# Optimization experiments

Measured on AMD Instinct MI355X. Metric: run time of the kernel, lower is better.

The kernel has to match this reference:

```python
import jax, jax.numpy as jnp
import numpy as np

N_EMBD = 1024
N_HEAD = 16
HEAD_DIM = N_EMBD // N_HEAD


def setup_inputs() -> dict:
    key = jax.random.key(0)
    k1, k2, k3 = jax.random.split(key, 3)
    x = jax.random.normal(k1, (2, 2048, N_EMBD), dtype=jnp.float32)
    # torch nn.Linear(in, out) weight has shape (out, in); y = x @ W.T
    w_qkv = jax.random.normal(k2, (3 * N_EMBD, N_EMBD), dtype=jnp.float32) * (1.0 / np.sqrt(N_EMBD))
    w_proj = jax.random.normal(k3, (N_EMBD, N_EMBD), dtype=jnp.float32) * (1.0 / np.sqrt(N_EMBD))
    return {"x": x, "w_qkv": w_qkv, "w_proj": w_proj}


def reference(x, w_qkv, w_proj):
    B, T, C = x.shape
    qkv = jnp.einsum('btc,dc->btd', x, w_qkv)  # [B,T,3C]
    q, k, v = jnp.split(qkv, 3, axis=2)
    # [B,H,T,hd]
    q = q.reshape(B, T, N_HEAD, HEAD_DIM).transpose(0, 2, 1, 3)
    k = k.reshape(B, T, N_HEAD, HEAD_DIM).transpose(0, 2, 1, 3)
    v = v.reshape(B, T, N_HEAD, HEAD_DIM).transpose(0, 2, 1, 3)
    att = jnp.einsum('bhqd,bhkd->bhqk', q, k) / jnp.sqrt(jnp.float32(HEAD_DIM))
    causal = jnp.tril(jnp.ones((T, T), dtype=bool))  # [T,T]
    att = jnp.where(causal[None, None], att, -jnp.inf)
    att = jax.nn.softmax(att, axis=-1)
    y = jnp.einsum('bhqk,bhkd->bhqd', att, v)
    y = y.transpose(0, 2, 1, 3).reshape(B, T, C)
    return jnp.einsum('btc,dc->btd', y, w_proj)
```

## Files before the change

kernel.cpp:

```cpp
#include <hip/hip_runtime.h>
#include <stdint.h>


typedef unsigned short u16;
typedef __bf16 bf16_t;
typedef bf16_t bf16x8 __attribute__((ext_vector_type(8)));
typedef float f32x4 __attribute__((ext_vector_type(4)));
typedef float f32x16 __attribute__((ext_vector_type(16)));

__device__ __forceinline__ u16 f2bf(float f) {
  return __builtin_bit_cast(u16, (bf16_t)f);
}

__device__ __forceinline__ float hexp2(float x) {
  float r;
  asm("v_exp_f32 %0, %1" : "=v"(r) : "v"(x));
  return r;
}
__device__ __forceinline__ uint32_t cvtpk(float lo, float hi) {
  uint32_t d;
  asm("v_cvt_pk_bf16_f32 %0, %1, %2" : "=v"(d) : "v"(lo), "v"(hi));
  return d;
}
__device__ __forceinline__ void plswap(uint32_t& a, uint32_t& b) {
  asm("v_permlane32_swap_b32 %0, %1" : "+v"(a), "+v"(b));
}

template<int CC>
__device__ __forceinline__ bf16x8 mkPfrag(const float* p) {
  uint32_t A1 = cvtpk(p[8 * CC + 0], p[8 * CC + 1]);
  uint32_t A2 = cvtpk(p[8 * CC + 2], p[8 * CC + 3]);
  uint32_t B1 = cvtpk(p[8 * CC + 4], p[8 * CC + 5]);
  uint32_t B2 = cvtpk(p[8 * CC + 6], p[8 * CC + 7]);
  plswap(A1, B1);
  plswap(A2, B2);
  union { uint32_t u[4]; bf16x8 v; } r;
  r.u[0] = A1; r.u[1] = A2; r.u[2] = B1; r.u[3] = B2;
  return r.v;
}

__device__ __forceinline__ void gload_lds16(const void* g, void* l) {
  __builtin_amdgcn_global_load_lds(
      (const __attribute__((address_space(1))) uint32_t*)(uint64_t)g,
      (__attribute__((address_space(3))) uint32_t*)(uint32_t)(uint64_t)l,
      16, 0, 0);
}

__global__ void cast_all(const float* __restrict__ x, const float* __restrict__ wq,
                         const float* __restrict__ wp, u16* __restrict__ xb,
                         u16* __restrict__ wqb, u16* __restrict__ wpb) {
  int i = blockIdx.x * blockDim.x + threadIdx.x;
  const float* s; u16* d; int off;
  if (i < 1048576)            { s = x;  d = xb;  off = i; }
  else if (i < 1048576 + 786432) { s = wq; d = wqb; off = i - 1048576; }
  else                        { s = wp; d = wpb; off = i - (1048576 + 786432); }
  float4 f = reinterpret_cast<const float4*>(s)[off];
  ushort4 o;
  o.x = f2bf(f.x); o.y = f2bf(f.y); o.z = f2bf(f.z); o.w = f2bf(f.w);
  reinterpret_cast<ushort4*>(d)[off] = o;
}

template<int MODE>
__global__ void gemm_bt(const u16* __restrict__ A, const u16* __restrict__ Bm,
                        u16* __restrict__ qb, u16* __restrict__ kb, u16* __restrict__ vb,
                        float* __restrict__ outf) {
  __shared__ __attribute__((aligned(16))) u16 SMEM[2 * 128 * 64];
  const int tid = threadIdx.x;
  const int lane = tid & 63;
  const int w = tid >> 6;
  const int wr = w >> 1, wc = w & 1;
  const int g = lane >> 4, r = lane & 15;
  const int tn = blockIdx.x, tm = blockIdx.y;

  f32x4 acc[4][4] = {};

  const char* Ab = (const char*)(A + (size_t)tm * 128 * 1024);
  const char* Bb = (const char*)(Bm + (size_t)tn * 128 * 1024);
  char* AsB = (char*)SMEM;
  char* BsB = AsB + 16384;

  for (int k0 = 0; k0 < 1024; k0 += 64) {
#pragma unroll
    for (int i = 0; i < 4; ++i) {
      const int L = (i * 256 + tid) * 16;
      const int row = L >> 7;
      const int colb = (L & 127) ^ ((row & 7) << 4);
      gload_lds16(Ab + (size_t)row * 2048 + k0 * 2 + colb, AsB + L);
      gload_lds16(Bb + (size_t)row * 2048 + k0 * 2 + colb, BsB + L);
    }
    __syncthreads();
#pragma unroll
    for (int kk = 0; kk < 2; ++kk) {
      bf16x8 a[4], b[4];
#pragma unroll
      for (int m = 0; m < 4; ++m) {
        const int rowA = wr * 64 + m * 16 + r;
        const int kbyt = (kk * 64 + g * 16) ^ ((rowA & 7) << 4);
        a[m] = *(const bf16x8*)(AsB + rowA * 128 + kbyt);
      }
#pragma unroll
      for (int n = 0; n < 4; ++n) {
        const int rowB = wc * 64 + n * 16 + r;
        const int kbyt = (kk * 64 + g * 16) ^ ((rowB & 7) << 4);
        b[n] = *(const bf16x8*)(BsB + rowB * 128 + kbyt);
      }
      __builtin_amdgcn_s_setprio(1);
#pragma unroll
      for (int m = 0; m < 4; ++m)
#pragma unroll
        for (int n = 0; n < 4; ++n)
          acc[m][n] = __builtin_amdgcn_mfma_f32_16x16x32_bf16(a[m], b[n], acc[m][n], 0, 0, 0);
      __builtin_amdgcn_s_setprio(0);
    }
    __syncthreads();
  }

  const int mrow0 = tm * 128 + wr * 64;
  const int ncol0 = tn * 128 + wc * 64;

  if (MODE == 1) {
#pragma unroll
    for (int m = 0; m < 4; ++m)
#pragma unroll
      for (int n = 0; n < 4; ++n) {
        const int nc = ncol0 + n * 16 + r;
#pragma unroll
        for (int j = 0; j < 4; ++j) {
          const int mr = mrow0 + m * 16 + g * 4 + j;
          outf[(size_t)mr * 1024 + nc] = acc[m][n][j];
        }
      }
  } else {
    const int sel = (blockIdx.x * 128) >> 10;
    const float qscl = (sel == 0) ? 0.18033688f : 1.0f;
    if (sel < 2) {
      u16* dst = (sel == 0) ? qb : kb;
#pragma unroll
      for (int m = 0; m < 4; ++m)
#pragma unroll
        for (int n = 0; n < 4; ++n) {
          const int nc = (ncol0 + n * 16 + r) & 1023;
          const int h = nc >> 6, d = nc & 63;
#pragma unroll
          for (int j = 0; j < 4; ++j) {
            const int mr = mrow0 + m * 16 + g * 4 + j;
            const int bb = mr >> 11, t = mr & 2047;
            dst[((size_t)(bb * 16 + h) * 2048 + t) * 64 + d] = f2bf(acc[m][n][j] * qscl);
          }
        }
    } else {
      u16* Wv = SMEM + w * 4096;
#pragma unroll
      for (int m = 0; m < 4; ++m)
#pragma unroll
        for (int n = 0; n < 4; ++n) {
          const int dl = n * 16 + r;
          uint32_t lo = cvtpk(acc[m][n][0], acc[m][n][1]);
          uint32_t hi2 = cvtpk(acc[m][n][2], acc[m][n][3]);
          char* p = (char*)Wv + dl * 128 + ((m * 32 + g * 8) ^ ((dl & 7) << 4));
          *(uint32_t*)p = lo;
          *(uint32_t*)(p + 4) = hi2;
        }
      asm volatile("s_waitcnt lgkmcnt(0)" ::: "memory");
      __builtin_amdgcn_sched_barrier(0);
      const int hh = (ncol0 - 2048) >> 6;
      const int t0 = mrow0 & 2047;
      const int bb2 = mrow0 >> 11;
      u16* vdst = vb + ((size_t)(bb2 * 16 + hh) * 64) * 2048 + t0;
#pragma unroll
      for (int rd = 0; rd < 8; ++rd) {
        const int dl = rd * 8 + (lane >> 3);
        const int tb = lane & 7;
        const char* src = (char*)Wv + dl * 128 + ((tb ^ (dl & 7)) << 4);
        *(uint4*)(vdst + (size_t)dl * 2048 + tb * 8) = *(const uint4*)src;
      }
    }
  }
}

__global__ __launch_bounds__(256, 2)
void attn_fwd(const u16* __restrict__ qb, const u16* __restrict__ kb,
              const u16* __restrict__ vb, u16* __restrict__ yb) {
  __shared__ __attribute__((aligned(16))) u16 KV[2][2][64 * 64];
  __shared__ __attribute__((aligned(16))) float Linv[4][32];
  const int tid = threadIdx.x;
  const int lane = tid & 63;
  const int w = tid >> 6;
  const int hi = lane >> 5;
  const int q5 = lane & 31;
  const int hi4 = hi * 4;
  const int bh = blockIdx.x;
  const int bb = bh >> 4, h = bh & 15;
  const int base = (blockIdx.y + bh) & 15;
  const int a = (base < 8) ? 2 * base : 31 - 2 * base;
  const int qb0 = a * 128;
  const int qw = qb0 + w * 32;
  const int qg = qw + q5;

  const char* Kb = (const char*)(kb + (size_t)bh * (2048 * 64));
  const char* Vb = (const char*)(vb + (size_t)bh * (64 * 2048));
  const u16* Q = qb + (size_t)bh * (2048 * 64);

  bf16x8 qf[4];
#pragma unroll
  for (int f = 0; f < 4; ++f)
    qf[f] = *(const bf16x8*)(&Q[(size_t)qg * 64 + f * 16 + hi * 8]);

  f32x16 o0 = {}, o1 = {};
  float psum = 0.0f;

  const int nt = (qw >> 6) + 1;
  const int ntmax = (qb0 >> 6) + 2;
  const int swz = (q5 & 7) << 4;

  auto stage = [&](int k0, int buf) {
#pragma unroll
    for (int i = 0; i < 2; ++i) {
      const int L = (i * 256 + tid) * 16;
      const int row = L >> 7;
      const int colb = (L & 127) ^ ((row & 7) << 4);
      gload_lds16(Kb + (size_t)(k0 + row) * 128 + colb, (char*)KV[buf][0] + L);
      gload_lds16(Vb + (size_t)row * 4096 + (size_t)k0 * 2 + colb,
                  (char*)KV[buf][1] + L);
    }
  };

  auto compute = [&](int t, int k0, const char* KsB, const char* VsB) {
    f32x16 s0 = {}, s1 = {};
    __builtin_amdgcn_s_setprio(1);
#pragma unroll
    for (int f = 0; f < 4; ++f) {
      const int cb = f * 32 + hi * 16;
      bf16x8 ka0 = *(const bf16x8*)(KsB + q5 * 128 + (cb ^ swz));
      bf16x8 ka1 = *(const bf16x8*)(KsB + (32 + q5) * 128 + (cb ^ swz));
      s0 = __builtin_amdgcn_mfma_f32_32x32x16_bf16(ka0, qf[f], s0, 0, 0, 0);
      s1 = __builtin_amdgcn_mfma_f32_32x32x16_bf16(ka1, qf[f], s1, 0, 0, 0);
    }
    __builtin_amdgcn_s_setprio(0);

    float p0[16], p1[16];
    if (t == nt - 1) {
#pragma unroll
      for (int i = 0; i < 16; ++i) {
        const int kl = (i & 3) + 8 * (i >> 2) + hi4;
        float e0 = hexp2(s0[i]);
        float e1 = hexp2(s1[i]);
        p0[i] = (k0 + kl <= qg) ? e0 : 0.0f;
        p1[i] = (k0 + 32 + kl <= qg) ? e1 : 0.0f;
        psum += p0[i] + p1[i];
      }
    } else {
#pragma unroll
      for (int i = 0; i < 16; ++i) {
        p0[i] = hexp2(s0[i]);
        p1[i] = hexp2(s1[i]);
        psum += p0[i] + p1[i];
      }
    }

    bf16x8 pf0 = mkPfrag<0>(p0);
    bf16x8 pf1 = mkPfrag<1>(p0);
    bf16x8 pf2 = mkPfrag<0>(p1);
    bf16x8 pf3 = mkPfrag<1>(p1);

    __builtin_amdgcn_s_setprio(1);
#pragma unroll
    for (int c = 0; c < 4; ++c) {
      const int cb = c * 32 + hi * 16;
      bf16x8 v0f = *(const bf16x8*)(VsB + q5 * 128 + (cb ^ swz));
      bf16x8 v1f = *(const bf16x8*)(VsB + (32 + q5) * 128 + (cb ^ swz));
      const bf16x8 pf = (c == 0) ? pf0 : (c == 1) ? pf1 : (c == 2) ? pf2 : pf3;
      o0 = __builtin_amdgcn_mfma_f32_32x32x16_bf16(pf, v0f, o0, 0, 0, 0);
      o1 = __builtin_amdgcn_mfma_f32_32x32x16_bf16(pf, v1f, o1, 0, 0, 0);
    }
    __builtin_amdgcn_s_setprio(0);
  };

  stage(0, 0);
  int t = 0;
  while (true) {
    const int k0n = (t + 1 < ntmax) ? (t + 1) * 64 : 0;
    stage(k0n, (t + 1) & 1);
    asm volatile("s_waitcnt vmcnt(4)" ::: "memory");
    __builtin_amdgcn_s_barrier();
    __builtin_amdgcn_sched_barrier(0);
    if (t < nt) compute(t, t * 64, (const char*)KV[t & 1][0], (const char*)KV[t & 1][1]);
    __builtin_amdgcn_sched_barrier(0);
    __builtin_amdgcn_s_barrier();
    if (++t >= ntmax) break;
  }

  const float tot = psum + __shfl_xor(psum, 32);
  if (lane < 32) Linv[w][q5] = 1.0f / tot;
  asm volatile("s_waitcnt lgkmcnt(0)" ::: "memory");
  __builtin_amdgcn_sched_barrier(0);
  f32x4 lv[4];
#pragma unroll
  for (int r2 = 0; r2 < 4; ++r2)
    lv[r2] = *(const f32x4*)(&Linv[w][r2 * 8 + hi4]);

#pragma unroll
  for (int reg = 0; reg < 16; ++reg) {
    const int r4 = reg & 3, r2 = reg >> 2;
    const float li = lv[r2][r4];
    const int trow = qw + r4 + 8 * r2 + hi4;
    const size_t bpos = ((size_t)(bb * 2048 + trow)) * 1024 + h * 64 + q5;
    yb[bpos]      = f2bf(o0[reg] * li);
    yb[bpos + 32] = f2bf(o1[reg] * li);
  }
}

extern "C" void kernel_launch(void* const* d_in, const int* in_sizes, int n_in,
                              void* d_out, int out_size, void* d_ws, size_t ws_size,
                              hipStream_t stream) {
  const float* x     = (const float*)d_in[0];
  const float* wqkv  = (const float*)d_in[1];
  const float* wproj = (const float*)d_in[2];
  float* out = (float*)d_out;
  char* ws = (char*)d_ws;
  u16* xb     = (u16*)(ws + (size_t)(0u  << 20));
  u16* wqkvb  = (u16*)(ws + (size_t)(8u  << 20));
  u16* wprojb = (u16*)(ws + (size_t)(14u << 20));
  u16* qb     = (u16*)(ws + (size_t)(16u << 20));
  u16* kb     = (u16*)(ws + (size_t)(24u << 20));
  u16* vb     = (u16*)(ws + (size_t)(32u << 20));
  u16* yb     = (u16*)(ws + (size_t)(40u << 20));

  cast_all<<<8192, 256, 0, stream>>>(x, wqkv, wproj, xb, wqkvb, wprojb);

  gemm_bt<0><<<dim3(24, 32), 256, 0, stream>>>(xb, wqkvb, qb, kb, vb, nullptr);
  attn_fwd<<<dim3(32, 16), 256, 0, stream>>>(qb, kb, vb, yb);
  gemm_bt<1><<<dim3(8, 32), 256, 0, stream>>>(yb, wprojb, nullptr, nullptr, nullptr, out);
}
```

Before: 95.72 us.

## Use 128-key KV phases in attention and smaller M tile for projection GEMM

Attention now stages 128-key K and V tiles per phase and skips fully masked 32-key sub-blocks per wave, halving the number of barrier-synchronised iterations. The projection GEMM gains a BM=64 template variant with a doubled grid to improve CU occupancy. The larger LDS buffers (64 KB per block) could constrain occupancy, and the per-sub-block causal branching adds control flow.

Result: faster. 93.40 us (-2.4%).

```diff
diff --git a/kernel.cpp b/kernel.cpp
--- a/kernel.cpp
+++ b/kernel.cpp
@@ -60,38 +60,46 @@
   reinterpret_cast<ushort4*>(d)[off] = o;
 }
 
-template<int MODE>
+template<int MODE, int BM>
 __global__ void gemm_bt(const u16* __restrict__ A, const u16* __restrict__ Bm,
                         u16* __restrict__ qb, u16* __restrict__ kb, u16* __restrict__ vb,
                         float* __restrict__ outf) {
-  __shared__ __attribute__((aligned(16))) u16 SMEM[2 * 128 * 64];
+  constexpr int NF = (BM == 128) ? 4 : 2;
+  __shared__ __attribute__((aligned(16))) u16 SMEM[BM * 64 + 128 * 64];
   const int tid = threadIdx.x;
   const int lane = tid & 63;
   const int w = tid >> 6;
-  const int wr = w >> 1, wc = w & 1;
+  const int wr = (BM == 128) ? (w >> 1) : 0;
+  const int wc = (BM == 128) ? (w & 1) : w;
   const int g = lane >> 4, r = lane & 15;
   const int tn = blockIdx.x, tm = blockIdx.y;
 
-  f32x4 acc[4][4] = {};
-
-  const char* Ab = (const char*)(A + (size_t)tm * 128 * 1024);
+  f32x4 acc[4][NF] = {};
+
+  const char* Ab = (const char*)(A + (size_t)tm * BM * 1024);
   const char* Bb = (const char*)(Bm + (size_t)tn * 128 * 1024);
   char* AsB = (char*)SMEM;
-  char* BsB = AsB + 16384;
+  char* BsB = AsB + BM * 128;
 
   for (int k0 = 0; k0 < 1024; k0 += 64) {
+#pragma unroll
+    for (int i = 0; i < BM / 32; ++i) {
+      const int L = (i * 256 + tid) * 16;
+      const int row = L >> 7;
+      const int colb = (L & 127) ^ ((row & 7) << 4);
+      gload_lds16(Ab + (size_t)row * 2048 + k0 * 2 + colb, AsB + L);
+    }
 #pragma unroll
     for (int i = 0; i < 4; ++i) {
       const int L = (i * 256 + tid) * 16;
       const int row = L >> 7;
       const int colb = (L & 127) ^ ((row & 7) << 4);
-      gload_lds16(Ab + (size_t)row * 2048 + k0 * 2 + colb, AsB + L);
       gload_lds16(Bb + (size_t)row * 2048 + k0 * 2 + colb, BsB + L);
     }
     __syncthreads();
 #pragma unroll
     for (int kk = 0; kk < 2; ++kk) {
-      bf16x8 a[4], b[4];
+      bf16x8 a[4], b[NF];
 #pragma unroll
       for (int m = 0; m < 4; ++m) {
         const int rowA = wr * 64 + m * 16 + r;
@@ -99,8 +107,8 @@
         a[m] = *(const bf16x8*)(AsB + rowA * 128 + kbyt);
       }
 #pragma unroll
-      for (int n = 0; n < 4; ++n) {
-        const int rowB = wc * 64 + n * 16 + r;
+      for (int n = 0; n < NF; ++n) {
+        const int rowB = wc * (NF * 16) + n * 16 + r;
         const int kbyt = (kk * 64 + g * 16) ^ ((rowB & 7) << 4);
         b[n] = *(const bf16x8*)(BsB + rowB * 128 + kbyt);
       }
@@ -108,21 +116,21 @@
 #pragma unroll
       for (int m = 0; m < 4; ++m)
 #pragma unroll
-        for (int n = 0; n < 4; ++n)
+        for (int n = 0; n < NF; ++n)
           acc[m][n] = __builtin_amdgcn_mfma_f32_16x16x32_bf16(a[m], b[n], acc[m][n], 0, 0, 0);
       __builtin_amdgcn_s_setprio(0);
     }
     __syncthreads();
   }
 
-  const int mrow0 = tm * 128 + wr * 64;
-  const int ncol0 = tn * 128 + wc * 64;
+  const int mrow0 = tm * BM + wr * 64;
+  const int ncol0 = tn * 128 + wc * (NF * 16);
 
   if (MODE == 1) {
 #pragma unroll
     for (int m = 0; m < 4; ++m)
 #pragma unroll
-      for (int n = 0; n < 4; ++n) {
+      for (int n = 0; n < NF; ++n) {
         const int nc = ncol0 + n * 16 + r;
 #pragma unroll
         for (int j = 0; j < 4; ++j) {
@@ -130,7 +138,7 @@
           outf[(size_t)mr * 1024 + nc] = acc[m][n][j];
         }
       }
-  } else {
+  } else if (MODE == 0) {
     const int sel = (blockIdx.x * 128) >> 10;
     const float qscl = (sel == 0) ? 0.18033688f : 1.0f;
     if (sel < 2) {
@@ -138,7 +146,7 @@
 #pragma unroll
       for (int m = 0; m < 4; ++m)
 #pragma unroll
-        for (int n = 0; n < 4; ++n) {
+        for (int n = 0; n < NF; ++n) {
           const int nc = (ncol0 + n * 16 + r) & 1023;
           const int h = nc >> 6, d = nc & 63;
 #pragma unroll
@@ -153,7 +161,7 @@
 #pragma unroll
       for (int m = 0; m < 4; ++m)
 #pragma unroll
-        for (int n = 0; n < 4; ++n) {
+        for (int n = 0; n < NF; ++n) {
           const int dl = n * 16 + r;
           uint32_t lo = cvtpk(acc[m][n][0], acc[m][n][1]);
           uint32_t hi2 = cvtpk(acc[m][n][2], acc[m][n][3]);
@@ -181,7 +189,8 @@
 __global__ __launch_bounds__(256, 2)
 void attn_fwd(const u16* __restrict__ qb, const u16* __restrict__ kb,
               const u16* __restrict__ vb, u16* __restrict__ yb) {
-  __shared__ __attribute__((aligned(16))) u16 KV[2][2][64 * 64];
+  __shared__ __attribute__((aligned(16))) u16 Ks[2][128 * 64];
+  __shared__ __attribute__((aligned(16))) u16 Vs[2][64 * 128];
   __shared__ __attribute__((aligned(16))) float Linv[4][32];
   const int tid = threadIdx.x;
   const int lane = tid & 63;
@@ -209,85 +218,87 @@
   f32x16 o0 = {}, o1 = {};
   float psum = 0.0f;
 
-  const int nt = (qw >> 6) + 1;
-  const int ntmax = (qb0 >> 6) + 2;
-  const int swz = (q5 & 7) << 4;
-
-  auto stage = [&](int k0, int buf) {
-#pragma unroll
-    for (int i = 0; i < 2; ++i) {
+  const int nph = a + 1;
+  const int swzK = (q5 & 7) << 4;
+  const int swzV = (q5 & 15) << 4;
+
+  auto stage = [&](int p, int buf) {
+#pragma unroll
+    for (int i = 0; i < 4; ++i) {
       const int L = (i * 256 + tid) * 16;
       const int row = L >> 7;
       const int colb = (L & 127) ^ ((row & 7) << 4);
-      gload_lds16(Kb + (size_t)(k0 + row) * 128 + colb, (char*)KV[buf][0] + L);
-      gload_lds16(Vb + (size_t)row * 4096 + (size_t)k0 * 2 + colb,
-                  (char*)KV[buf][1] + L);
+      gload_lds16(Kb + ((size_t)p * 128 + row) * 128 + colb, (char*)Ks[buf] + L);
+    }
+#pragma unroll
+    for (int i = 0; i < 4; ++i) {
+      const int L = (i * 256 + tid) * 16;
+      const int row = L >> 8;
+      const int colb = (L & 255) ^ ((row & 15) << 4);
+      gload_lds16(Vb + (size_t)row * 4096 + (size_t)p * 256 + colb, (char*)Vs[buf] + L);
     }
   };
 
-  auto compute = [&](int t, int k0, const char* KsB, const char* VsB) {
-    f32x16 s0 = {}, s1 = {};
-    __builtin_amdgcn_s_setprio(1);
-#pragma unroll
-    for (int f = 0; f < 4; ++f) {
-      const int cb = f * 32 + hi * 16;
-      bf16x8 ka0 = *(const bf16x8*)(KsB + q5 * 128 + (cb ^ swz));
-      bf16x8 ka1 = *(const bf16x8*)(KsB + (32 + q5) * 128 + (cb ^ swz));
-      s0 = __builtin_amdgcn_mfma_f32_32x32x16_bf16(ka0, qf[f], s0, 0, 0, 0);
-      s1 = __builtin_amdgcn_mfma_f32_32x32x16_bf16(ka1, qf[f], s1, 0, 0, 0);
-    }
-    __builtin_amdgcn_s_setprio(0);
-
-    float p0[16], p1[16];
-    if (t == nt - 1) {
-#pragma unroll
-      for (int i = 0; i < 16; ++i) {
-        const int kl = (i & 3) + 8 * (i >> 2) + hi4;
-        float e0 = hexp2(s0[i]);
-        float e1 = hexp2(s1[i]);
-        p0[i] = (k0 + kl <= qg) ? e0 : 0.0f;
-        p1[i] = (k0 + 32 + kl <= qg) ? e1 : 0.0f;
-        psum += p0[i] + p1[i];
-      }
-    } else {
-#pragma unroll
-      for (int i = 0; i < 16; ++i) {
-        p0[i] = hexp2(s0[i]);
-        p1[i] = hexp2(s1[i]);
-        psum += p0[i] + p1[i];
-      }
-    }
-
-    bf16x8 pf0 = mkPfrag<0>(p0);
-    bf16x8 pf1 = mkPfrag<1>(p0);
-    bf16x8 pf2 = mkPfrag<0>(p1);
-    bf16x8 pf3 = mkPfrag<1>(p1);
-
-    __builtin_amdgcn_s_setprio(1);
-#pragma unroll
-    for (int c = 0; c < 4; ++c) {
-      const int cb = c * 32 + hi * 16;
-      bf16x8 v0f = *(const bf16x8*)(VsB + q5 * 128 + (cb ^ swz));
-      bf16x8 v1f = *(const bf16x8*)(VsB + (32 + q5) * 128 + (cb ^ swz));
-      const bf16x8 pf = (c == 0) ? pf0 : (c == 1) ? pf1 : (c == 2) ? pf2 : pf3;
-      o0 = __builtin_amdgcn_mfma_f32_32x32x16_bf16(pf, v0f, o0, 0, 0, 0);
-      o1 = __builtin_amdgcn_mfma_f32_32x32x16_bf16(pf, v1f, o1, 0, 0, 0);
-    }
-    __builtin_amdgcn_s_setprio(0);
+  auto compute = [&](int p, const char* KsB, const char* VsB) {
+#pragma unroll
+    for (int hh = 0; hh < 4; ++hh) {
+      const int kh = p * 128 + hh * 32;
+      if (kh <= qw + 31) {
+        f32x16 s = {};
+        __builtin_amdgcn_s_setprio(1);
+#pragma unroll
+        for (int f = 0; f < 4; ++f) {
+          bf16x8 ka = *(const bf16x8*)(KsB + (hh * 32 + q5) * 128 + ((f * 32 + hi * 16) ^ swzK));
+          s = __builtin_amdgcn_mfma_f32_32x32x16_bf16(ka, qf[f], s, 0, 0, 0);
+        }
+        __builtin_amdgcn_s_setprio(0);
+
+        float pv[16];
+        if (kh + 31 > qw) {
+#pragma unroll
+          for (int i = 0; i < 16; ++i) {
+            const int kl = (i & 3) + 8 * (i >> 2) + hi4;
+            float e = hexp2(s[i]);
+            pv[i] = (kh + kl <= qg) ? e : 0.0f;
+            psum += pv[i];
+          }
+        } else {
+#pragma unroll
+          for (int i = 0; i < 16; ++i) {
+            pv[i] = hexp2(s[i]);
+            psum += pv[i];
+          }
+        }
+
+        bf16x8 pf0 = mkPfrag<0>(pv);
+        bf16x8 pf1 = mkPfrag<1>(pv);
+
+        __builtin_amdgcn_s_setprio(1);
+#pragma unroll
+        for (int c = 0; c < 2; ++c) {
+          const int cc = hh * 2 + c;
+          const int cb = cc * 32 + hi * 16;
+          bf16x8 v0f = *(const bf16x8*)(VsB + q5 * 256 + (cb ^ swzV));
+          bf16x8 v1f = *(const bf16x8*)(VsB + (32 + q5) * 256 + (cb ^ swzV));
+          const bf16x8 pf = c ? pf1 : pf0;
+          o0 = __builtin_amdgcn_mfma_f32_32x32x16_bf16(pf, v0f, o0, 0, 0, 0);
+          o1 = __builtin_amdgcn_mfma_f32_32x32x16_bf16(pf, v1f, o1, 0, 0, 0);
+        }
+        __builtin_amdgcn_s_setprio(0);
+      }
+    }
   };
 
   stage(0, 0);
-  int t = 0;
-  while (true) {
-    const int k0n = (t + 1 < ntmax) ? (t + 1) * 64 : 0;
-    stage(k0n, (t + 1) & 1);
-    asm volatile("s_waitcnt vmcnt(4)" ::: "memory");
+  for (int t = 0; t < nph; ++t) {
+    const int pn = (t + 1 < nph) ? t + 1 : 0;
+    stage(pn, (t + 1) & 1);
+    asm volatile("s_waitcnt vmcnt(8)" ::: "memory");
     __builtin_amdgcn_s_barrier();
     __builtin_amdgcn_sched_barrier(0);
-    if (t < nt) compute(t, t * 64, (const char*)KV[t & 1][0], (const char*)KV[t & 1][1]);
+    compute(t, (const char*)Ks[t & 1], (const char*)Vs[t & 1]);
     __builtin_amdgcn_sched_barrier(0);
     __builtin_amdgcn_s_barrier();
-    if (++t >= ntmax) break;
   }
 
   const float tot = psum + __shfl_xor(psum, 32);
@@ -328,7 +339,7 @@
 
   cast_all<<<8192, 256, 0, stream>>>(x, wqkv, wproj, xb, wqkvb, wprojb);
 
-  gemm_bt<0><<<dim3(24, 32), 256, 0, stream>>>(xb, wqkvb, qb, kb, vb, nullptr);
+  gemm_bt<0, 128><<<dim3(24, 32), 256, 0, stream>>>(xb, wqkvb, qb, kb, vb, nullptr);
   attn_fwd<<<dim3(32, 16), 256, 0, stream>>>(qb, kb, vb, yb);
-  gemm_bt<1><<<dim3(8, 32), 256, 0, stream>>>(yb, wprojb, nullptr, nullptr, nullptr, out);
-}
+  gemm_bt<1, 64><<<dim3(8, 64), 256, 0, stream>>>(yb, wprojb, nullptr, nullptr, nullptr, out);
+}
```
